# Kernel optimization log

Measured on AMD Instinct MI355X. Metric: run time of the kernel, lower is better.

Reference implementation:

```python
import jax, jax.numpy as jnp
import numpy as np

EPS = 1e-5

def layer_norm(x, w, b):
    # Faithful to the module: divides by (sqrt(var) + eps), NOT sqrt(var + eps).
    m = jnp.mean(x, axis=-1, keepdims=True)
    v = jnp.mean((x - m) ** 2, axis=-1, keepdims=True)
    return (x - m) / (jnp.sqrt(v) + EPS) * w + b

def setup_inputs() -> dict:
    key = jax.random.key(0)
    B, S, E, H, F = 8, 2048, 512, 8, 2048
    ks = jax.random.split(key, 8)
    def lin(k, fin, fout):
        k1, k2 = jax.random.split(k)
        return (jax.random.normal(k1, (fin, fout), jnp.float32) * (1.0 / np.sqrt(fin)),
                jax.random.normal(k2, (fout,), jnp.float32) * 0.01)
    WQ, bQ = lin(ks[0], E, E)
    WK, bK = lin(ks[1], E, E)
    WV, bV = lin(ks[2], E, E)
    WY, bY = lin(ks[3], E, E)
    W1, b1 = lin(ks[4], E, F)
    W2, b2 = lin(ks[5], F, E)
    x = jax.random.normal(ks[6], (B, S, E), jnp.float32)
    return {
        "x": x,
        "WQ": WQ, "bQ": bQ, "WK": WK, "bK": bK, "WV": WV, "bV": bV,
        "WY": WY, "bY": bY,
        "ln1_w": jnp.ones((E,), jnp.float32), "ln1_b": jnp.zeros((E,), jnp.float32),
        "W1": W1, "b1": b1, "W2": W2, "b2": b2,
        "ln2_w": jnp.ones((E,), jnp.float32), "ln2_b": jnp.zeros((E,), jnp.float32),
    }

def attention(x, WQ, bQ, WK, bK, WV, bV, WY, bY, num_heads=8):
    B, S, E = x.shape
    D = E // num_heads  # head_size
    def split(t):  # (B,S,E) -> (B,H,S,D)
        return t.reshape(B, S, num_heads, D).transpose(0, 2, 1, 3)
    q = split(x @ WQ + bQ)
    k = split(x @ WK + bK)
    v = split(x @ WV + bV)
    scores = jnp.einsum('bhsd,bhtd->bhst', q, k) / jnp.sqrt(jnp.float32(D))
    w = jax.nn.softmax(scores, axis=-1)  # full (B,H,S,S) attention matrix, as in original
    y = jnp.einsum('bhst,bhtd->bhsd', w, v)
    y = y.transpose(0, 2, 1, 3).reshape(B, S, E)  # merge heads
    return y @ WY + bY

def reference(x, WQ, bQ, WK, bK, WV, bV, WY, bY, ln1_w, ln1_b, W1, b1, W2, b2, ln2_w, ln2_b):
    attn_out = attention(x, WQ, bQ, WK, bK, WV, bV, WY, bY)
    h = layer_norm(x + attn_out, ln1_w, ln1_b)  # post-norm
    mlp = jax.nn.gelu(h @ W1 + b1, approximate=False) @ W2 + b2
    out = layer_norm(h + mlp, ln2_w, ln2_b)
    return out
```

## Files before the change

kernel.cpp:

```cpp
#include <hip/hip_runtime.h>
#include <hip/hip_bf16.h>
#include <cstdint>

typedef unsigned short u16;
typedef __bf16 __attribute__((ext_vector_type(8))) bf16x8;
typedef float __attribute__((ext_vector_type(4))) f32x4;

#define B_ 8
#define S_ 2048
#define E_ 512
#define H_ 8
#define D_ 64
#define F_ 2048
#define MTOT (B_ * S_)
#define QSCALE 0.18033688011112042f
#define MFIX 12.0f

static __device__ __forceinline__ float bf2f(u16 u) {
    union { uint32_t i; float f; } x;
    x.i = ((uint32_t)u) << 16;
    return x.f;
}
static __device__ __forceinline__ u16 f2bf(float f) {
    __hip_bfloat16 h = __float2bfloat16(f);
    return *reinterpret_cast<u16*>(&h);
}
static __device__ __forceinline__ float fast_exp2(float x) {
    float r;
    asm("v_exp_f32 %0, %1" : "=v"(r) : "v"(x));
    return r;
}
static __device__ __forceinline__ float fast_exp2_neg(float x) {
    float r;
    asm("v_exp_f32 %0, -%1" : "=v"(r) : "v"(x));
    return r;
}
static __device__ __forceinline__ float fast_rcp(float x) {
    float r;
    asm("v_rcp_f32 %0, %1" : "=v"(r) : "v"(x));
    return r;
}
static __device__ __forceinline__ uint32_t cvt_pk_bf16(float a, float b) {
    uint32_t r;
    asm("v_cvt_pk_bf16_f32 %0, %1, %2" : "=v"(r) : "v"(a), "v"(b));
    return r;
}
static __device__ __forceinline__ float fast_gelu(float v) {
    float x2 = v * v;
    float w = v * fmaf(0.10294818f, x2, 2.3022066f);
    float e = fast_exp2_neg(w);
    return v * fast_rcp(1.0f + e);
}

__global__ __launch_bounds__(256) void prep(const float* __restrict__ x,
                                            u16* __restrict__ xb,
                                            const float* __restrict__ WQ,
                                            const float* __restrict__ WK,
                                            const float* __restrict__ WV,
                                            const float* __restrict__ WY,
                                            const float* __restrict__ W1,
                                            const float* __restrict__ W2,
                                            u16* __restrict__ WQKVT,
                                            u16* __restrict__ WYT,
                                            u16* __restrict__ W1T,
                                            u16* __restrict__ W2T,
                                            const float* __restrict__ bQ,
                                            const float* __restrict__ bK,
                                            const float* __restrict__ bV,
                                            float* __restrict__ bqkv) {
    const int bid = blockIdx.x;
    const int tid = threadIdx.x;
    if (bid < 4096) {
        int i = bid * 256 + tid;
        const float4* p = reinterpret_cast<const float4*>(x) + (size_t)i * 2;
        float4 a = p[0], b = p[1];
        uint4 o;
        o.x = cvt_pk_bf16(a.x, a.y);
        o.y = cvt_pk_bf16(a.z, a.w);
        o.z = cvt_pk_bf16(b.x, b.y);
        o.w = cvt_pk_bf16(b.z, b.w);
        *reinterpret_cast<uint4*>(xb + (size_t)i * 8) = o;
        return;
    }
    int r = bid - 4096;
    if (r >= 3072) {
        int i = (r - 3072) * 256 + tid;
        if (i < 1536) bqkv[i] = i < 512 ? bQ[i] : (i < 1024 ? bK[i - 512] : bV[i - 1024]);
        return;
    }
    __shared__ float tile[32][33];
    const float* src;
    u16* dst;
    int K, N, bx, by;
    if (r < 1024) {
        int w = r >> 8, idx = r & 255;
        bx = idx & 15; by = idx >> 4; K = 512; N = 512;
        src = w == 0 ? WQ : (w == 1 ? WK : (w == 2 ? WV : WY));
        dst = (w == 3) ? WYT : (WQKVT + (size_t)w * 512 * 512);
    } else if (r < 2048) {
        int idx = r - 1024;
        bx = idx & 63; by = idx >> 6; K = 512; N = 2048;
        src = W1; dst = W1T;
    } else {
        int idx = r - 2048;
        bx = idx & 15; by = idx >> 4; K = 2048; N = 512;
        src = W2; dst = W2T;
    }
    const int tx = tid & 31, ty = tid >> 5;
    int n0 = bx * 32, k0 = by * 32;
    for (int i = ty; i < 32; i += 8)
        tile[i][tx] = src[(size_t)(k0 + i) * N + n0 + tx];
    __syncthreads();
    for (int i = ty; i < 32; i += 8)
        dst[(size_t)(n0 + i) * K + k0 + tx] = f2bf(tile[tx][i]);
}

template <int ACT, int SPLIT>
__global__ __launch_bounds__(512) void gemm_bt(const u16* __restrict__ A,
                                               const u16* __restrict__ BT,
                                               const float* __restrict__ bias,
                                               void* __restrict__ Cv,
                                               u16* __restrict__ Vtg,
                                               int Mdim, int Ndim, int Kdim) {
    __shared__ u16 As[128 * 64];
    __shared__ u16 Bs[128 * 64];
    const int tid = threadIdx.x;
    const int wave = tid >> 6, lane = tid & 63;
    const int lr = lane & 15, lg = lane >> 4;

    const int gx = gridDim.x;
    int lin = blockIdx.y * gx + blockIdx.x;
    const int nwg = gx * gridDim.y;
    if ((nwg & 7) == 0) {
        int cpx = nwg >> 3;
        lin = (lin & 7) * cpx + (lin >> 3);
    }
    const int m0 = (lin / gx) * 128, n0 = (lin % gx) * 128;
    const int wrow = (wave >> 2) * 64, wcol = (wave & 3) * 32;

    f32x4 acc[4][2];
#pragma unroll
    for (int i = 0; i < 4; i++)
#pragma unroll
        for (int j = 0; j < 2; j++) acc[i][j] = (f32x4){0.f, 0.f, 0.f, 0.f};

    const int stagerow = tid >> 3;
    const int stagechunk = (tid & 7) * 8;

    for (int k0 = 0; k0 < Kdim; k0 += 64) {
        __syncthreads();
#pragma unroll
        for (int it = 0; it < 2; ++it) {
            int row = stagerow + it * 64;
            const u16* ga = A + (size_t)(m0 + row) * Kdim + k0 + stagechunk;
            const u16* gb = BT + (size_t)(n0 + row) * Kdim + k0 + stagechunk;
            __builtin_amdgcn_global_load_lds(
                (const __attribute__((address_space(1))) void*)ga,
                (__attribute__((address_space(3))) void*)(As + row * 64 + stagechunk),
                16, 0, 0);
            __builtin_amdgcn_global_load_lds(
                (const __attribute__((address_space(1))) void*)gb,
                (__attribute__((address_space(3))) void*)(Bs + row * 64 + stagechunk),
                16, 0, 0);
        }
        __syncthreads();
#pragma unroll
        for (int kk = 0; kk < 64; kk += 32) {
            bf16x8 af[4], bfr[2];
#pragma unroll
            for (int i = 0; i < 4; i++)
                af[i] = *reinterpret_cast<const bf16x8*>(As + (wrow + i * 16 + lr) * 64 + kk + lg * 8);
#pragma unroll
            for (int j = 0; j < 2; j++)
                bfr[j] = *reinterpret_cast<const bf16x8*>(Bs + (wcol + j * 16 + lr) * 64 + kk + lg * 8);
#pragma unroll
            for (int i = 0; i < 4; i++)
#pragma unroll
                for (int j = 0; j < 2; j++)
                    acc[i][j] = __builtin_amdgcn_mfma_f32_16x16x32_bf16(af[i], bfr[j], acc[i][j], 0, 0, 0);
        }
    }

#pragma unroll
    for (int j = 0; j < 2; j++) {
        int col = n0 + wcol + j * 16 + lr;
        float bv = bias[col];
        int seg = col >> 9, c2 = col & 511;
#pragma unroll
        for (int i = 0; i < 4; i++) {
            int rowb = m0 + wrow + i * 16 + lg * 4;
            float vv[4];
#pragma unroll
            for (int r = 0; r < 4; r++) {
                float v = acc[i][j][r] + bv;
                if (ACT == 1) v = fast_gelu(v);
                if (SPLIT) { if (seg == 0) v *= QSCALE; }
                vv[r] = v;
            }
            uint32_t p01 = cvt_pk_bf16(vv[0], vv[1]);
            uint32_t p23 = cvt_pk_bf16(vv[2], vv[3]);
            if (SPLIT) {
                if (seg == 2) {
                    int bb = rowb >> 11, s = rowb & 2047;
                    *reinterpret_cast<uint2*>(Vtg + ((size_t)bb * E_ + c2) * S_ + s) =
                        (uint2){p01, p23};
                } else {
                    u16* dst = (u16*)Cv + (size_t)seg * ((size_t)MTOT * 512) + (size_t)rowb * 512 + c2;
                    dst[0] = (u16)p01; dst[512] = (u16)(p01 >> 16);
                    dst[1024] = (u16)p23; dst[1536] = (u16)(p23 >> 16);
                }
            } else {
                u16* dst = (u16*)Cv + (size_t)rowb * Ndim + col;
                dst[0] = (u16)p01; dst[Ndim] = (u16)(p01 >> 16);
                dst[2 * (size_t)Ndim] = (u16)p23; dst[3 * (size_t)Ndim] = (u16)(p23 >> 16);
            }
        }
    }
}

__global__ __launch_bounds__(512, 4) void attn_fwd(const u16* __restrict__ Q,
                                                   const u16* __restrict__ K,
                                                   const u16* __restrict__ Vt,
                                                   u16* __restrict__ Y) {
    __shared__ u16 Ks[64 * 64];
    __shared__ u16 Vs[64 * 64];
    __shared__ u16 Ps[8][32 * 64];
    const int tid = threadIdx.x;
    const int wave = tid >> 6, lane = tid & 63;
    const int lr = lane & 15, lg = lane >> 4;
    const int swq = lr & 7;
    const int lin = blockIdx.x;
    const int idx = lin >> 3;
    const int bh = (lin & 7) + 8 * (idx >> 3);
    const int s0 = (idx & 7) * 256;
    const int b = bh >> 3, h = bh & 7;
    const size_t headoff = ((size_t)b * S_) * E_ + (size_t)h * D_;
    const size_t vtoff = (size_t)bh * D_ * S_;
    const int qb = s0 + wave * 32;

    bf16x8 qf[2][2];
#pragma unroll
    for (int qh = 0; qh < 2; qh++) {
        const u16* qrow = Q + headoff + (size_t)(qb + qh * 16 + lr) * E_;
        qf[qh][0] = *reinterpret_cast<const bf16x8*>(qrow + lg * 8);
        qf[qh][1] = *reinterpret_cast<const bf16x8*>(qrow + 32 + lg * 8);
    }
    f32x4 o[2][4];
#pragma unroll
    for (int qh = 0; qh < 2; qh++)
#pragma unroll
        for (int j = 0; j < 4; j++) o[qh][j] = (f32x4){0.f, 0.f, 0.f, 0.f};
    float lrow[2] = {0.f, 0.f};

    const int r8 = lane >> 3, c8 = lane & 7;
    const int srcch = c8 ^ r8;
    const int strow = wave * 8 + r8;
    u16* pw = Ps[wave];

    auto STAGE_K = [&](int t) {
        const u16* gk = K + headoff + (size_t)(t * 64 + strow) * E_ + srcch * 8;
        __builtin_amdgcn_global_load_lds(
            (const __attribute__((address_space(1))) void*)gk,
            (__attribute__((address_space(3))) void*)(Ks + strow * 64 + c8 * 8), 16, 0, 0);
    };
    auto STAGE_V = [&](int t) {
        const u16* gv = Vt + vtoff + (size_t)strow * S_ + t * 64 + srcch * 8;
        __builtin_amdgcn_global_load_lds(
            (const __attribute__((address_space(1))) void*)gv,
            (__attribute__((address_space(3))) void*)(Vs + strow * 64 + c8 * 8), 16, 0, 0);
    };

    STAGE_K(0);
    STAGE_V(0);
    __syncthreads();

    for (int t = 0; t < S_ / 64; ++t) {
        f32x4 sc[2][4];
        __builtin_amdgcn_s_setprio(1);
#pragma unroll
        for (int j = 0; j < 4; j++) {
            int row = j * 16 + lr;
            bf16x8 k0 = *reinterpret_cast<const bf16x8*>(Ks + row * 64 + ((lg ^ swq) << 3));
            bf16x8 k1 = *reinterpret_cast<const bf16x8*>(Ks + row * 64 + (((4 + lg) ^ swq) << 3));
#pragma unroll
            for (int qh = 0; qh < 2; qh++) {
                f32x4 a = (f32x4){-MFIX, -MFIX, -MFIX, -MFIX};
                a = __builtin_amdgcn_mfma_f32_16x16x32_bf16(k0, qf[qh][0], a, 0, 0, 0);
                a = __builtin_amdgcn_mfma_f32_16x16x32_bf16(k1, qf[qh][1], a, 0, 0, 0);
                sc[qh][j] = a;
            }
        }
        __builtin_amdgcn_s_setprio(0);
        __syncthreads();
        if (t + 1 < S_ / 64) STAGE_K(t + 1);

#pragma unroll
        for (int qh = 0; qh < 2; qh++) {
            float rs = 0.f;
            int prow = qh * 16 + lr;
#pragma unroll
            for (int j = 0; j < 4; j++) {
                float p0 = fast_exp2(sc[qh][j][0]);
                float p1 = fast_exp2(sc[qh][j][1]);
                float p2 = fast_exp2(sc[qh][j][2]);
                float p3 = fast_exp2(sc[qh][j][3]);
                rs += (p0 + p1) + (p2 + p3);
                uint2 pk;
                pk.x = cvt_pk_bf16(p0, p1);
                pk.y = cvt_pk_bf16(p2, p3);
                int cc = (j * 2 + (lg >> 1)) ^ swq;
                *reinterpret_cast<uint2*>(pw + prow * 64 + cc * 8 + (lg & 1) * 4) = pk;
            }
            rs += __shfl_xor(rs, 16);
            rs += __shfl_xor(rs, 32);
            lrow[qh] += rs;
        }

        __builtin_amdgcn_s_setprio(1);
#pragma unroll
        for (int kk = 0; kk < 2; kk++) {
            int pc = ((kk * 4 + lg) ^ swq) << 3;
            bf16x8 ap0 = *reinterpret_cast<const bf16x8*>(pw + lr * 64 + pc);
            bf16x8 ap1 = *reinterpret_cast<const bf16x8*>(pw + (16 + lr) * 64 + pc);
#pragma unroll
            for (int j = 0; j < 4; j++) {
                int row = j * 16 + lr;
                bf16x8 bv = *reinterpret_cast<const bf16x8*>(Vs + row * 64 + (((kk * 4 + lg) ^ (row & 7)) << 3));
                o[0][j] = __builtin_amdgcn_mfma_f32_16x16x32_bf16(ap0, bv, o[0][j], 0, 0, 0);
                o[1][j] = __builtin_amdgcn_mfma_f32_16x16x32_bf16(ap1, bv, o[1][j], 0, 0, 0);
            }
        }
        __builtin_amdgcn_s_setprio(0);
        __syncthreads();
        if (t + 1 < S_ / 64) STAGE_V(t + 1);
    }

#pragma unroll
    for (int qh = 0; qh < 2; qh++) {
        float rl[4];
#pragma unroll
        for (int r = 0; r < 4; r++) {
            float lq = __shfl(lrow[qh], (lane & 48) | (lg * 4 + r));
            rl[r] = fast_rcp(lq);
        }
#pragma unroll
        for (int j = 0; j < 4; j++) {
            uint32_t p01 = cvt_pk_bf16(o[qh][j][0] * rl[0], o[qh][j][1] * rl[1]);
            uint32_t p23 = cvt_pk_bf16(o[qh][j][2] * rl[2], o[qh][j][3] * rl[3]);
            u16* dst = Y + headoff + (size_t)(qb + qh * 16 + lg * 4) * E_ + j * 16 + lr;
            dst[0] = (u16)p01; dst[E_] = (u16)(p01 >> 16);
            dst[2 * E_] = (u16)p23; dst[3 * E_] = (u16)(p23 >> 16);
        }
    }
}

template <int F32OUT>
__global__ __launch_bounds__(256) void resid_ln(const u16* __restrict__ X,
                                                const u16* __restrict__ Yres,
                                                const float* __restrict__ W,
                                                const float* __restrict__ Bb,
                                                void* __restrict__ H) {
    const int tid = threadIdx.x;
    const int wave = tid >> 6, lane = tid & 63;
    const size_t row = (size_t)blockIdx.x * 4 + wave;
    uint4 xa = *reinterpret_cast<const uint4*>(X + row * E_ + lane * 8);
    uint4 ya = *reinterpret_cast<const uint4*>(Yres + row * E_ + lane * 8);
    const u16* xu = reinterpret_cast<const u16*>(&xa);
    const u16* yu = reinterpret_cast<const u16*>(&ya);
    float v[8];
    float s = 0.f, sq = 0.f;
#pragma unroll
    for (int e = 0; e < 8; e++) {
        v[e] = bf2f(xu[e]) + bf2f(yu[e]);
        s += v[e];
        sq += v[e] * v[e];
    }
#pragma unroll
    for (int msk = 1; msk < 64; msk <<= 1) {
        s += __shfl_xor(s, msk);
        sq += __shfl_xor(sq, msk);
    }
    float mean = s * (1.f / E_);
    float var = fmaxf(sq * (1.f / E_) - mean * mean, 0.f);
    float rstd = 1.f / (sqrtf(var) + 1e-5f);
    const float4* wr = reinterpret_cast<const float4*>(W + lane * 8);
    const float4* br = reinterpret_cast<const float4*>(Bb + lane * 8);
    float4 w0 = wr[0], w1 = wr[1], b0 = br[0], b1 = br[1];
    float wv[8] = {w0.x, w0.y, w0.z, w0.w, w1.x, w1.y, w1.z, w1.w};
    float bv[8] = {b0.x, b0.y, b0.z, b0.w, b1.x, b1.y, b1.z, b1.w};
    float out[8];
#pragma unroll
    for (int e = 0; e < 8; e++) out[e] = (v[e] - mean) * rstd * wv[e] + bv[e];
    if (F32OUT) {
        float4* hw = reinterpret_cast<float4*>((float*)H + row * E_ + lane * 8);
        hw[0] = (float4){out[0], out[1], out[2], out[3]};
        hw[1] = (float4){out[4], out[5], out[6], out[7]};
    } else {
        uint4 ob;
        ob.x = cvt_pk_bf16(out[0], out[1]);
        ob.y = cvt_pk_bf16(out[2], out[3]);
        ob.z = cvt_pk_bf16(out[4], out[5]);
        ob.w = cvt_pk_bf16(out[6], out[7]);
        *reinterpret_cast<uint4*>((u16*)H + row * E_ + lane * 8) = ob;
    }
}

extern "C" void kernel_launch(void* const* d_in, const int* in_sizes, int n_in,
                              void* d_out, int out_size, void* d_ws, size_t ws_size,
                              hipStream_t stream) {
    const float* x = (const float*)d_in[0];
    const float* WQ = (const float*)d_in[1];
    const float* bQ = (const float*)d_in[2];
    const float* WK = (const float*)d_in[3];
    const float* bK = (const float*)d_in[4];
    const float* WV = (const float*)d_in[5];
    const float* bV = (const float*)d_in[6];
    const float* WY = (const float*)d_in[7];
    const float* bY = (const float*)d_in[8];
    const float* ln1w = (const float*)d_in[9];
    const float* ln1b = (const float*)d_in[10];
    const float* W1 = (const float*)d_in[11];
    const float* b1 = (const float*)d_in[12];
    const float* W2 = (const float*)d_in[13];
    const float* b2 = (const float*)d_in[14];
    const float* ln2w = (const float*)d_in[15];
    const float* ln2b = (const float*)d_in[16];

    char* ws = (char*)d_ws;
    const size_t MB = 1024 * 1024;
    u16* WQKVT = (u16*)(ws);
    u16* WYT = (u16*)(ws + (size_t)1536 * 1024);
    u16* W1T = (u16*)(ws + 2 * MB);
    u16* W2T = (u16*)(ws + 4 * MB);
    float* bqkv = (float*)(ws + 6 * MB);
    u16* xb   = (u16*)(ws + 7 * MB);
    u16* Qb   = (u16*)(ws + 23 * MB);
    u16* Kb   = (u16*)(ws + 39 * MB);
    u16* Vtg  = (u16*)(ws + 55 * MB);
    u16* Yb   = (u16*)(ws + 71 * MB);
    u16* attnb = Vtg;
    u16* hb   = Qb;
    u16* hid  = Kb;
    u16* m2b  = xb;

    dim3 blk(256);
    dim3 gblk(512);
    prep<<<dim3(7174), blk, 0, stream>>>(x, xb, WQ, WK, WV, WY, W1, W2,
                                         WQKVT, WYT, W1T, W2T, bQ, bK, bV, bqkv);
    gemm_bt<0, 1><<<dim3(12, 128), gblk, 0, stream>>>(xb, WQKVT, bqkv, Qb, Vtg, MTOT, 1536, 512);
    attn_fwd<<<dim3(512), dim3(512), 0, stream>>>(Qb, Kb, Vtg, Yb);
    gemm_bt<0, 0><<<dim3(4, 128), gblk, 0, stream>>>(Yb, WYT, bY, attnb, nullptr, MTOT, 512, 512);
    resid_ln<0><<<dim3(4096), blk, 0, stream>>>(xb, attnb, ln1w, ln1b, hb);
    gemm_bt<1, 0><<<dim3(16, 128), gblk, 0, stream>>>(hb, W1T, b1, hid, nullptr, MTOT, 2048, 512);
    gemm_bt<0, 0><<<dim3(4, 128), gblk, 0, stream>>>(hid, W2T, b2, m2b, nullptr, MTOT, 512, 2048);
    resid_ln<1><<<dim3(4096), blk, 0, stream>>>(hb, m2b, ln2w, ln2b, (float*)d_out);
}
```

Baseline: 283.5 us.

## Switch attention to 32x32x16 MFMA and keep P in registers via permlane swap

Rewrites the attention inner loop to use 32x32x16 bf16 MFMA tiles with the key block as the A operand, so the score accumulator layout can be converted directly into the P operand using v_permlane32_swap. This removes the per-wave shared-memory P buffer along with its LDS writes and reads, and reduces the row-sum shuffles. The trade-offs are larger accumulator register footprints (f32x16), which may raise register pressure under the 512-thread launch bound, and a scalar epilogue that shuffles the row sum once per output row.

```diff
diff --git a/kernel.cpp b/kernel.cpp
--- a/kernel.cpp
+++ b/kernel.cpp
@@ -5,6 +5,7 @@
 typedef unsigned short u16;
 typedef __bf16 __attribute__((ext_vector_type(8))) bf16x8;
 typedef float __attribute__((ext_vector_type(4))) f32x4;
+typedef float __attribute__((ext_vector_type(16))) f32x16;
 
 #define B_ 8
 #define S_ 2048
@@ -224,38 +225,34 @@
                                                    u16* __restrict__ Y) {
     __shared__ u16 Ks[64 * 64];
     __shared__ u16 Vs[64 * 64];
-    __shared__ u16 Ps[8][32 * 64];
     const int tid = threadIdx.x;
     const int wave = tid >> 6, lane = tid & 63;
-    const int lr = lane & 15, lg = lane >> 4;
-    const int swq = lr & 7;
+    const int l31 = lane & 31, h = lane >> 5;
     const int lin = blockIdx.x;
     const int idx = lin >> 3;
     const int bh = (lin & 7) + 8 * (idx >> 3);
     const int s0 = (idx & 7) * 256;
-    const int b = bh >> 3, h = bh & 7;
-    const size_t headoff = ((size_t)b * S_) * E_ + (size_t)h * D_;
+    const int b = bh >> 3, hd = bh & 7;
+    const size_t headoff = ((size_t)b * S_) * E_ + (size_t)hd * D_;
     const size_t vtoff = (size_t)bh * D_ * S_;
     const int qb = s0 + wave * 32;
-
-    bf16x8 qf[2][2];
-#pragma unroll
-    for (int qh = 0; qh < 2; qh++) {
-        const u16* qrow = Q + headoff + (size_t)(qb + qh * 16 + lr) * E_;
-        qf[qh][0] = *reinterpret_cast<const bf16x8*>(qrow + lg * 8);
-        qf[qh][1] = *reinterpret_cast<const bf16x8*>(qrow + 32 + lg * 8);
-    }
-    f32x4 o[2][4];
-#pragma unroll
-    for (int qh = 0; qh < 2; qh++)
-#pragma unroll
-        for (int j = 0; j < 4; j++) o[qh][j] = (f32x4){0.f, 0.f, 0.f, 0.f};
-    float lrow[2] = {0.f, 0.f};
+    const int sw31 = l31 & 7;
+
+    bf16x8 qf[4];
+    {
+        const u16* qrow = Q + headoff + (size_t)(qb + l31) * E_ + h * 8;
+#pragma unroll
+        for (int db = 0; db < 4; db++)
+            qf[db] = *reinterpret_cast<const bf16x8*>(qrow + db * 16);
+    }
+    f32x16 o0 = {0.f, 0.f, 0.f, 0.f, 0.f, 0.f, 0.f, 0.f,
+                 0.f, 0.f, 0.f, 0.f, 0.f, 0.f, 0.f, 0.f};
+    f32x16 o1 = o0;
+    float lrow = 0.f;
 
     const int r8 = lane >> 3, c8 = lane & 7;
     const int srcch = c8 ^ r8;
     const int strow = wave * 8 + r8;
-    u16* pw = Ps[wave];
 
     auto STAGE_K = [&](int t) {
         const u16* gk = K + headoff + (size_t)(t * 64 + strow) * E_ + srcch * 8;
@@ -275,60 +272,76 @@
     __syncthreads();
 
     for (int t = 0; t < S_ / 64; ++t) {
-        f32x4 sc[2][4];
+        f32x16 sc0 = {-MFIX, -MFIX, -MFIX, -MFIX, -MFIX, -MFIX, -MFIX, -MFIX,
+                      -MFIX, -MFIX, -MFIX, -MFIX, -MFIX, -MFIX, -MFIX, -MFIX};
+        f32x16 sc1 = sc0;
         __builtin_amdgcn_s_setprio(1);
 #pragma unroll
-        for (int j = 0; j < 4; j++) {
-            int row = j * 16 + lr;
-            bf16x8 k0 = *reinterpret_cast<const bf16x8*>(Ks + row * 64 + ((lg ^ swq) << 3));
-            bf16x8 k1 = *reinterpret_cast<const bf16x8*>(Ks + row * 64 + (((4 + lg) ^ swq) << 3));
-#pragma unroll
-            for (int qh = 0; qh < 2; qh++) {
-                f32x4 a = (f32x4){-MFIX, -MFIX, -MFIX, -MFIX};
-                a = __builtin_amdgcn_mfma_f32_16x16x32_bf16(k0, qf[qh][0], a, 0, 0, 0);
-                a = __builtin_amdgcn_mfma_f32_16x16x32_bf16(k1, qf[qh][1], a, 0, 0, 0);
-                sc[qh][j] = a;
-            }
+        for (int db = 0; db < 4; db++) {
+            int cc = ((db * 2 + h) ^ sw31) * 8;
+            bf16x8 a0 = *reinterpret_cast<const bf16x8*>(Ks + l31 * 64 + cc);
+            bf16x8 a1 = *reinterpret_cast<const bf16x8*>(Ks + (32 + l31) * 64 + cc);
+            sc0 = __builtin_amdgcn_mfma_f32_32x32x16_bf16(a0, qf[db], sc0, 0, 0, 0);
+            sc1 = __builtin_amdgcn_mfma_f32_32x32x16_bf16(a1, qf[db], sc1, 0, 0, 0);
         }
         __builtin_amdgcn_s_setprio(0);
         __syncthreads();
         if (t + 1 < S_ / 64) STAGE_K(t + 1);
 
-#pragma unroll
-        for (int qh = 0; qh < 2; qh++) {
-            float rs = 0.f;
-            int prow = qh * 16 + lr;
-#pragma unroll
-            for (int j = 0; j < 4; j++) {
-                float p0 = fast_exp2(sc[qh][j][0]);
-                float p1 = fast_exp2(sc[qh][j][1]);
-                float p2 = fast_exp2(sc[qh][j][2]);
-                float p3 = fast_exp2(sc[qh][j][3]);
-                rs += (p0 + p1) + (p2 + p3);
-                uint2 pk;
-                pk.x = cvt_pk_bf16(p0, p1);
-                pk.y = cvt_pk_bf16(p2, p3);
-                int cc = (j * 2 + (lg >> 1)) ^ swq;
-                *reinterpret_cast<uint2*>(pw + prow * 64 + cc * 8 + (lg & 1) * 4) = pk;
+        bf16x8 pa[4];
+        float rs = 0.f;
+#pragma unroll
+        for (int kh = 0; kh < 2; kh++) {
+#pragma unroll
+            for (int f = 0; f < 2; f++) {
+                float p0, p1, p2, p3, p4, p5, p6, p7;
+                if (kh == 0) {
+                    if (f == 0) {
+                        p0 = fast_exp2(sc0[0]); p1 = fast_exp2(sc0[1]);
+                        p2 = fast_exp2(sc0[2]); p3 = fast_exp2(sc0[3]);
+                        p4 = fast_exp2(sc0[4]); p5 = fast_exp2(sc0[5]);
+                        p6 = fast_exp2(sc0[6]); p7 = fast_exp2(sc0[7]);
+                    } else {
+                        p0 = fast_exp2(sc0[8]);  p1 = fast_exp2(sc0[9]);
+                        p2 = fast_exp2(sc0[10]); p3 = fast_exp2(sc0[11]);
+                        p4 = fast_exp2(sc0[12]); p5 = fast_exp2(sc0[13]);
+                        p6 = fast_exp2(sc0[14]); p7 = fast_exp2(sc0[15]);
+                    }
+                } else {
+                    if (f == 0) {
+                        p0 = fast_exp2(sc1[0]); p1 = fast_exp2(sc1[1]);
+                        p2 = fast_exp2(sc1[2]); p3 = fast_exp2(sc1[3]);
+                        p4 = fast_exp2(sc1[4]); p5 = fast_exp2(sc1[5]);
+                        p6 = fast_exp2(sc1[6]); p7 = fast_exp2(sc1[7]);
+                    } else {
+                        p0 = fast_exp2(sc1[8]);  p1 = fast_exp2(sc1[9]);
+                        p2 = fast_exp2(sc1[10]); p3 = fast_exp2(sc1[11]);
+                        p4 = fast_exp2(sc1[12]); p5 = fast_exp2(sc1[13]);
+                        p6 = fast_exp2(sc1[14]); p7 = fast_exp2(sc1[15]);
+                    }
+                }
+                rs += ((p0 + p1) + (p2 + p3)) + ((p4 + p5) + (p6 + p7));
+                uint32_t x0 = cvt_pk_bf16(p0, p1);
+                uint32_t x1 = cvt_pk_bf16(p2, p3);
+                uint32_t y0 = cvt_pk_bf16(p4, p5);
+                uint32_t y1 = cvt_pk_bf16(p6, p7);
+                asm("v_permlane32_swap_b32 %0, %1" : "+v"(x0), "+v"(y0));
+                asm("v_permlane32_swap_b32 %0, %1" : "+v"(x1), "+v"(y1));
+                uint4 av = {x0, x1, y0, y1};
+                pa[kh * 2 + f] = *reinterpret_cast<const bf16x8*>(&av);
             }
-            rs += __shfl_xor(rs, 16);
-            rs += __shfl_xor(rs, 32);
-            lrow[qh] += rs;
-        }
+        }
+        rs += __shfl_xor(rs, 32);
+        lrow += rs;
 
         __builtin_amdgcn_s_setprio(1);
 #pragma unroll
-        for (int kk = 0; kk < 2; kk++) {
-            int pc = ((kk * 4 + lg) ^ swq) << 3;
-            bf16x8 ap0 = *reinterpret_cast<const bf16x8*>(pw + lr * 64 + pc);
-            bf16x8 ap1 = *reinterpret_cast<const bf16x8*>(pw + (16 + lr) * 64 + pc);
-#pragma unroll
-            for (int j = 0; j < 4; j++) {
-                int row = j * 16 + lr;
-                bf16x8 bv = *reinterpret_cast<const bf16x8*>(Vs + row * 64 + (((kk * 4 + lg) ^ (row & 7)) << 3));
-                o[0][j] = __builtin_amdgcn_mfma_f32_16x16x32_bf16(ap0, bv, o[0][j], 0, 0, 0);
-                o[1][j] = __builtin_amdgcn_mfma_f32_16x16x32_bf16(ap1, bv, o[1][j], 0, 0, 0);
-            }
+        for (int s = 0; s < 4; s++) {
+            int cc = ((s * 2 + h) ^ sw31) * 8;
+            bf16x8 bv0 = *reinterpret_cast<const bf16x8*>(Vs + l31 * 64 + cc);
+            bf16x8 bv1 = *reinterpret_cast<const bf16x8*>(Vs + (32 + l31) * 64 + cc);
+            o0 = __builtin_amdgcn_mfma_f32_32x32x16_bf16(pa[s], bv0, o0, 0, 0, 0);
+            o1 = __builtin_amdgcn_mfma_f32_32x32x16_bf16(pa[s], bv1, o1, 0, 0, 0);
         }
         __builtin_amdgcn_s_setprio(0);
         __syncthreads();
@@ -336,21 +349,12 @@
     }
 
 #pragma unroll
-    for (int qh = 0; qh < 2; qh++) {
-        float rl[4];
-#pragma unroll
-        for (int r = 0; r < 4; r++) {
-            float lq = __shfl(lrow[qh], (lane & 48) | (lg * 4 + r));
-            rl[r] = fast_rcp(lq);
-        }
-#pragma unroll
-        for (int j = 0; j < 4; j++) {
-            uint32_t p01 = cvt_pk_bf16(o[qh][j][0] * rl[0], o[qh][j][1] * rl[1]);
-            uint32_t p23 = cvt_pk_bf16(o[qh][j][2] * rl[2], o[qh][j][3] * rl[3]);
-            u16* dst = Y + headoff + (size_t)(qb + qh * 16 + lg * 4) * E_ + j * 16 + lr;
-            dst[0] = (u16)p01; dst[E_] = (u16)(p01 >> 16);
-            dst[2 * E_] = (u16)p23; dst[3 * E_] = (u16)(p23 >> 16);
-        }
+    for (int r = 0; r < 16; r++) {
+        int q = (r & 3) + 8 * (r >> 2) + 4 * h;
+        float rl = fast_rcp(__shfl(lrow, q));
+        u16* dst = Y + headoff + (size_t)(qb + q) * E_ + l31;
+        dst[0] = f2bf(o0[r] * rl);
+        dst[32] = f2bf(o1[r] * rl);
     }
 }
 
```

After: 277.6 us, median of 3. 1.02x faster.
